# Kernel tuning notes

Hardware: AMD Instinct MI355X
Metric: run time of the kernel (lower is better)

## Reference

```python
import jax, jax.numpy as jnp
import numpy as np

NBITS = 1
GROUP_SIZE = 64
OUT_F = 4096
IN_F = 4096


def setup_inputs() -> dict:
    key = jax.random.key(0)
    k1, k2, k3, k4, k5 = jax.random.split(key, 5)
    x = jax.random.normal(k1, (8192, IN_F), dtype=jnp.float32)
    # packed 1-bit weights: 8 bits per byte, stored as int32 in [0,256)
    W_packed = jax.random.randint(k2, (OUT_F, IN_F // 8), 0, 256, dtype=jnp.int32)
    n_groups = OUT_F * IN_F // GROUP_SIZE
    scale = jax.random.uniform(k3, (n_groups, 1), dtype=jnp.float32) * 0.02 + 0.005
    zero = jax.random.normal(k4, (n_groups, 1), dtype=jnp.float32) * 0.5
    bias = jax.random.normal(k5, (OUT_F,), dtype=jnp.float32) * 0.02
    return {"x": x, "W_packed": W_packed, "scale": scale, "zero": zero, "bias": bias}


def _unpack_1bit(W_packed):
    # (out, in//8) int -> (out, in) float bits, bit 0 first within each byte
    bits = (W_packed[..., None] >> jnp.arange(8, dtype=jnp.int32)) & 1  # (out, in//8, 8)
    return bits.reshape(W_packed.shape[0], -1).astype(jnp.float32)      # (out, in)


def _dequantise(W_packed, scale, zero):
    W_q = _unpack_1bit(W_packed)                       # (out, in)
    W_grouped = W_q.reshape(-1, GROUP_SIZE)            # (n_groups, group_size), axis=1 grouping
    W_hat = (W_grouped - zero) * scale                 # per-group affine dequant
    return W_hat.reshape(OUT_F, IN_F)


def reference(x, W_packed, scale, zero, bias):
    W_hat = _dequantise(W_packed, scale, zero)
    # F.linear: x @ W_hat.T + bias
    return jnp.dot(x, W_hat.T) + bias
```

## Files before the change

kernel.cpp:

```cpp
#include <hip/hip_runtime.h>
#include <hip/hip_bf16.h>

#define IN_F   4096
#define OUT_F  4096

typedef __bf16 bf16;
typedef __attribute__((ext_vector_type(8))) __bf16 bf16x8;
typedef __attribute__((ext_vector_type(4))) __bf16 bf16x4;
typedef __attribute__((ext_vector_type(4))) float floatx4;

__global__ __launch_bounds__(256) void convert_x_kernel(
    const float* __restrict__ x, bf16* __restrict__ xb)
{
    const size_t i = (size_t)blockIdx.x * 256 + threadIdx.x;
    float4 v = ((const float4*)x)[i];
    bf16x4 b = { (bf16)v.x, (bf16)v.y, (bf16)v.z, (bf16)v.w };
    ((bf16x4*)xb)[i] = b;
}

__global__ __launch_bounds__(256) void dequant_w_kernel(
    const int* __restrict__ Wp, const float* __restrict__ scale,
    const float* __restrict__ zero, bf16* __restrict__ Wb)
{
    const int tid = blockIdx.x * 256 + threadIdx.x;
    const int n = tid >> 9;
    const int b = tid & 511;
    const int g = (n << 6) + (b >> 3);
    const float sc = scale[g];
    const float zp = zero[g];
    const bf16 hi = (bf16)((1.0f - zp) * sc);
    const bf16 lo = (bf16)((0.0f - zp) * sc);
    const int v = Wp[tid];
    bf16x8 w;
#pragma unroll
    for (int j = 0; j < 8; ++j) w[j] = ((v >> j) & 1) ? hi : lo;
    *(bf16x8*)&Wb[(size_t)tid * 8] = w;
}

__device__ __forceinline__ void gload_lds16(const void* g, void* l) {
    __builtin_amdgcn_global_load_lds(
        (const __attribute__((address_space(1))) unsigned int*)g,
        (__attribute__((address_space(3))) unsigned int*)l, 16, 0, 0);
}

__global__ __launch_bounds__(256) void bf16_gemm_bt_kernel(
    const bf16* __restrict__ A,
    const bf16* __restrict__ B,
    const float* __restrict__ bias,
    float* __restrict__ out)
{
    __shared__ __align__(16) bf16 as[128 * 64];
    __shared__ __align__(16) bf16 bs[128 * 64];

    const int t      = threadIdx.x;
    const int lane   = t & 63;
    const int wave   = t >> 6;
    const int lane16 = lane & 15;
    const int kq     = lane >> 4;
    const int wm     = wave >> 1;
    const int wn     = wave & 1;

    const int n0 = blockIdx.x * 128;
    const int m0 = blockIdx.y * 128;

    floatx4 acc[4][4];
#pragma unroll
    for (int i = 0; i < 4; ++i)
#pragma unroll
        for (int j = 0; j < 4; ++j)
            acc[i][j] = (floatx4){0.f, 0.f, 0.f, 0.f};

    const int srow8 = lane >> 3;
    const int sunit = lane & 7;

    for (int kt = 0; kt < IN_F / 64; ++kt) {
#pragma unroll
        for (int i = 0; i < 4; ++i) {
            const int row   = wave * 32 + i * 8 + srow8;
            const int gunit = sunit ^ (row & 7);
            gload_lds16(A + (size_t)(m0 + row) * IN_F + kt * 64 + gunit * 8,
                        &as[(wave * 32 + i * 8) * 64]);
            gload_lds16(B + (size_t)(n0 + row) * IN_F + kt * 64 + gunit * 8,
                        &bs[(wave * 32 + i * 8) * 64]);
        }
        __syncthreads();

#pragma unroll
        for (int ks = 0; ks < 2; ++ks) {
            const int u = ks * 4 + kq;
            bf16x8 af[4], bfr[4];
#pragma unroll
            for (int i = 0; i < 4; ++i) {
                const int r = wm * 64 + i * 16 + lane16;
                af[i] = *(const bf16x8*)&as[r * 64 + (u ^ (r & 7)) * 8];
            }
#pragma unroll
            for (int j = 0; j < 4; ++j) {
                const int r = wn * 64 + j * 16 + lane16;
                bfr[j] = *(const bf16x8*)&bs[r * 64 + (u ^ (r & 7)) * 8];
            }
#pragma unroll
            for (int i = 0; i < 4; ++i)
#pragma unroll
                for (int j = 0; j < 4; ++j)
                    acc[i][j] = __builtin_amdgcn_mfma_f32_16x16x32_bf16(
                        af[i], bfr[j], acc[i][j], 0, 0, 0);
        }
        __syncthreads();
    }

#pragma unroll
    for (int j = 0; j < 4; ++j) {
        const int col = n0 + wn * 64 + j * 16 + lane16;
        const float bv = bias[col];
#pragma unroll
        for (int i = 0; i < 4; ++i) {
            const int row = m0 + wm * 64 + i * 16 + kq * 4;
#pragma unroll
            for (int r = 0; r < 4; ++r)
                out[(size_t)(row + r) * OUT_F + col] = acc[i][j][r] + bv;
        }
    }
}

#define SA 72
#define SB 72
__global__ __launch_bounds__(256) void hqq_gemm_fused_kernel(
    const float* __restrict__ x, const int* __restrict__ Wp,
    const float* __restrict__ scale, const float* __restrict__ zero,
    const float* __restrict__ bias, float* __restrict__ out)
{
    __shared__ __align__(16) bf16 asmem[128 * SA];
    __shared__ __align__(16) bf16 bsmem[128 * SB];
    const int t = threadIdx.x, lane = t & 63, wave = t >> 6;
    const int lane16 = lane & 15, kq = lane >> 4;
    const int wm = wave >> 1, wn = wave & 1;
    const int n0 = blockIdx.x * 128, m0 = blockIdx.y * 128;
    floatx4 acc[4][4];
#pragma unroll
    for (int i = 0; i < 4; ++i)
#pragma unroll
        for (int j = 0; j < 4; ++j) acc[i][j] = (floatx4){0.f, 0.f, 0.f, 0.f};
    const int a_col4 = t & 15, a_row0 = t >> 4;
    const int b_nl = t >> 1, b_half = t & 1;
    for (int kt = 0; kt < IN_F / 64; ++kt) {
        const float* xp = x + (size_t)(m0 + a_row0) * IN_F + kt * 64 + a_col4 * 4;
#pragma unroll
        for (int p = 0; p < 8; ++p) {
            float4 v = *(const float4*)(xp + (size_t)(p * 16) * IN_F);
            bf16x4 b = { (bf16)v.x, (bf16)v.y, (bf16)v.z, (bf16)v.w };
            *(bf16x4*)&asmem[(a_row0 + p * 16) * SA + a_col4 * 4] = b;
        }
        {
            const int4 v = *(const int4*)(Wp + (size_t)(n0 + b_nl) * (IN_F / 8)
                                          + kt * 8 + b_half * 4);
            const int g = (n0 + b_nl) * (IN_F / 64) + kt;
            const float sc = scale[g], zp = zero[g];
            const bf16 hi = (bf16)((1.0f - zp) * sc), lo = (bf16)(0.0f - zp * sc);
            const int vals[4] = {v.x, v.y, v.z, v.w};
#pragma unroll
            for (int e = 0; e < 4; ++e) {
                bf16x8 w;
#pragma unroll
                for (int j = 0; j < 8; ++j) w[j] = ((vals[e] >> j) & 1) ? hi : lo;
                *(bf16x8*)&bsmem[b_nl * SB + b_half * 32 + e * 8] = w;
            }
        }
        __syncthreads();
#pragma unroll
        for (int ks = 0; ks < 2; ++ks) {
            bf16x8 af[4], bfr[4];
#pragma unroll
            for (int i = 0; i < 4; ++i)
                af[i] = *(const bf16x8*)&asmem[(wm * 64 + i * 16 + lane16) * SA + ks * 32 + kq * 8];
#pragma unroll
            for (int j = 0; j < 4; ++j)
                bfr[j] = *(const bf16x8*)&bsmem[(wn * 64 + j * 16 + lane16) * SB + ks * 32 + kq * 8];
#pragma unroll
            for (int i = 0; i < 4; ++i)
#pragma unroll
                for (int j = 0; j < 4; ++j)
                    acc[i][j] = __builtin_amdgcn_mfma_f32_16x16x32_bf16(af[i], bfr[j], acc[i][j], 0, 0, 0);
        }
        __syncthreads();
    }
#pragma unroll
    for (int j = 0; j < 4; ++j) {
        const int col = n0 + wn * 64 + j * 16 + lane16;
        const float bv = bias[col];
#pragma unroll
        for (int i = 0; i < 4; ++i) {
            const int row = m0 + wm * 64 + i * 16 + kq * 4;
#pragma unroll
            for (int r = 0; r < 4; ++r)
                out[(size_t)(row + r) * OUT_F + col] = acc[i][j][r] + bv;
        }
    }
}

extern "C" void kernel_launch(void* const* d_in, const int* in_sizes, int n_in,
                              void* d_out, int out_size, void* d_ws, size_t ws_size,
                              hipStream_t stream) {
    const float* x     = (const float*)d_in[0];
    const int*   Wp    = (const int*)d_in[1];
    const float* scale = (const float*)d_in[2];
    const float* zero  = (const float*)d_in[3];
    const float* bias  = (const float*)d_in[4];
    float*       out   = (float*)d_out;

    const int M = in_sizes[0] / IN_F;
    const size_t need = (size_t)M * IN_F * 2 + (size_t)OUT_F * IN_F * 2;

    if (ws_size >= need) {
        bf16* xb = (bf16*)d_ws;
        bf16* Wb = (bf16*)((char*)d_ws + (size_t)M * IN_F * 2);

        convert_x_kernel<<<(M * IN_F / 4) / 256, 256, 0, stream>>>(x, xb);
        dequant_w_kernel<<<(OUT_F * IN_F / 8) / 256, 256, 0, stream>>>(Wp, scale, zero, Wb);

        dim3 grid(OUT_F / 128, M / 128);
        bf16_gemm_bt_kernel<<<grid, 256, 0, stream>>>(xb, Wb, bias, out);
    } else {
        dim3 grid(OUT_F / 128, M / 128);
        hqq_gemm_fused_kernel<<<grid, 256, 0, stream>>>(x, Wp, scale, zero, bias, out);
    }
}
```

Before: 523.2 us.

## Switch GEMM to 32x32x16 MFMA and merge prep kernels into one launch

The bf16 GEMM inner loop now issues 32x32x16 MFMA instructions on 2x2 tiles per wave instead of 16x16x32 on 4x4 tiles. This needs fewer LDS fragment reads per k-step and fewer instructions to issue. The activation conversion and weight dequantisation kernels are merged into a single launch that branches on block index, saving one launch. The epilogue store mapping is rewritten for the 32x32 accumulator layout, and output stores are less contiguous per wave.

```diff
diff --git a/kernel.cpp b/kernel.cpp
--- a/kernel.cpp
+++ b/kernel.cpp
@@ -5,36 +5,36 @@
 #define OUT_F  4096
 
 typedef __bf16 bf16;
-typedef __attribute__((ext_vector_type(8))) __bf16 bf16x8;
-typedef __attribute__((ext_vector_type(4))) __bf16 bf16x4;
-typedef __attribute__((ext_vector_type(4))) float floatx4;
-
-__global__ __launch_bounds__(256) void convert_x_kernel(
-    const float* __restrict__ x, bf16* __restrict__ xb)
+typedef __attribute__((ext_vector_type(8)))  __bf16 bf16x8;
+typedef __attribute__((ext_vector_type(4)))  __bf16 bf16x4;
+typedef __attribute__((ext_vector_type(4)))  float  floatx4;
+typedef __attribute__((ext_vector_type(16))) float  floatx16;
+
+__global__ __launch_bounds__(256) void prep_kernel(
+    const float* __restrict__ x,  bf16* __restrict__ xb,
+    const int* __restrict__ Wp,   const float* __restrict__ scale,
+    const float* __restrict__ zero, bf16* __restrict__ Wb, int nxb)
 {
-    const size_t i = (size_t)blockIdx.x * 256 + threadIdx.x;
-    float4 v = ((const float4*)x)[i];
-    bf16x4 b = { (bf16)v.x, (bf16)v.y, (bf16)v.z, (bf16)v.w };
-    ((bf16x4*)xb)[i] = b;
-}
-
-__global__ __launch_bounds__(256) void dequant_w_kernel(
-    const int* __restrict__ Wp, const float* __restrict__ scale,
-    const float* __restrict__ zero, bf16* __restrict__ Wb)
-{
-    const int tid = blockIdx.x * 256 + threadIdx.x;
-    const int n = tid >> 9;
-    const int b = tid & 511;
-    const int g = (n << 6) + (b >> 3);
-    const float sc = scale[g];
-    const float zp = zero[g];
-    const bf16 hi = (bf16)((1.0f - zp) * sc);
-    const bf16 lo = (bf16)((0.0f - zp) * sc);
-    const int v = Wp[tid];
-    bf16x8 w;
-#pragma unroll
-    for (int j = 0; j < 8; ++j) w[j] = ((v >> j) & 1) ? hi : lo;
-    *(bf16x8*)&Wb[(size_t)tid * 8] = w;
+    if ((int)blockIdx.x < nxb) {
+        const size_t i = (size_t)blockIdx.x * 256 + threadIdx.x;
+        float4 v = ((const float4*)x)[i];
+        bf16x4 b = { (bf16)v.x, (bf16)v.y, (bf16)v.z, (bf16)v.w };
+        ((bf16x4*)xb)[i] = b;
+    } else {
+        const int tid = (blockIdx.x - nxb) * 256 + threadIdx.x;
+        const int n = tid >> 9;
+        const int b = tid & 511;
+        const int g = (n << 6) + (b >> 3);
+        const float sc = scale[g];
+        const float zp = zero[g];
+        const bf16 hi = (bf16)((1.0f - zp) * sc);
+        const bf16 lo = (bf16)((0.0f - zp) * sc);
+        const int v = Wp[tid];
+        bf16x8 w;
+#pragma unroll
+        for (int j = 0; j < 8; ++j) w[j] = ((v >> j) & 1) ? hi : lo;
+        *(bf16x8*)&Wb[(size_t)tid * 8] = w;
+    }
 }
 
 __device__ __forceinline__ void gload_lds16(const void* g, void* l) {
@@ -55,20 +55,21 @@
     const int t      = threadIdx.x;
     const int lane   = t & 63;
     const int wave   = t >> 6;
-    const int lane16 = lane & 15;
-    const int kq     = lane >> 4;
+    const int lane32 = lane & 31;
+    const int half   = lane >> 5;
     const int wm     = wave >> 1;
     const int wn     = wave & 1;
 
     const int n0 = blockIdx.x * 128;
     const int m0 = blockIdx.y * 128;
 
-    floatx4 acc[4][4];
-#pragma unroll
-    for (int i = 0; i < 4; ++i)
-#pragma unroll
-        for (int j = 0; j < 4; ++j)
-            acc[i][j] = (floatx4){0.f, 0.f, 0.f, 0.f};
+    floatx16 acc[2][2];
+#pragma unroll
+    for (int i = 0; i < 2; ++i)
+#pragma unroll
+        for (int j = 0; j < 2; ++j)
+#pragma unroll
+            for (int r = 0; r < 16; ++r) acc[i][j][r] = 0.f;
 
     const int srow8 = lane >> 3;
     const int sunit = lane & 7;
@@ -86,39 +87,41 @@
         __syncthreads();
 
 #pragma unroll
-        for (int ks = 0; ks < 2; ++ks) {
-            const int u = ks * 4 + kq;
-            bf16x8 af[4], bfr[4];
-#pragma unroll
-            for (int i = 0; i < 4; ++i) {
-                const int r = wm * 64 + i * 16 + lane16;
+        for (int s = 0; s < 4; ++s) {
+            const int u = s * 2 + half;
+            bf16x8 af[2], bfr[2];
+#pragma unroll
+            for (int i = 0; i < 2; ++i) {
+                const int r = wm * 64 + i * 32 + lane32;
                 af[i] = *(const bf16x8*)&as[r * 64 + (u ^ (r & 7)) * 8];
             }
 #pragma unroll
-            for (int j = 0; j < 4; ++j) {
-                const int r = wn * 64 + j * 16 + lane16;
+            for (int j = 0; j < 2; ++j) {
+                const int r = wn * 64 + j * 32 + lane32;
                 bfr[j] = *(const bf16x8*)&bs[r * 64 + (u ^ (r & 7)) * 8];
             }
 #pragma unroll
-            for (int i = 0; i < 4; ++i)
-#pragma unroll
-                for (int j = 0; j < 4; ++j)
-                    acc[i][j] = __builtin_amdgcn_mfma_f32_16x16x32_bf16(
+            for (int i = 0; i < 2; ++i)
+#pragma unroll
+                for (int j = 0; j < 2; ++j)
+                    acc[i][j] = __builtin_amdgcn_mfma_f32_32x32x16_bf16(
                         af[i], bfr[j], acc[i][j], 0, 0, 0);
         }
         __syncthreads();
     }
 
 #pragma unroll
-    for (int j = 0; j < 4; ++j) {
-        const int col = n0 + wn * 64 + j * 16 + lane16;
+    for (int j = 0; j < 2; ++j) {
+        const int col = n0 + wn * 64 + j * 32 + lane32;
         const float bv = bias[col];
 #pragma unroll
-        for (int i = 0; i < 4; ++i) {
-            const int row = m0 + wm * 64 + i * 16 + kq * 4;
-#pragma unroll
-            for (int r = 0; r < 4; ++r)
-                out[(size_t)(row + r) * OUT_F + col] = acc[i][j][r] + bv;
+        for (int i = 0; i < 2; ++i) {
+            const int rowbase = m0 + wm * 64 + i * 32 + 4 * half;
+#pragma unroll
+            for (int reg = 0; reg < 16; ++reg) {
+                const int row = rowbase + (reg & 3) + 8 * (reg >> 2);
+                out[(size_t)row * OUT_F + col] = acc[i][j][reg] + bv;
+            }
         }
     }
 }
@@ -215,8 +218,9 @@
         bf16* xb = (bf16*)d_ws;
         bf16* Wb = (bf16*)((char*)d_ws + (size_t)M * IN_F * 2);
 
-        convert_x_kernel<<<(M * IN_F / 4) / 256, 256, 0, stream>>>(x, xb);
-        dequant_w_kernel<<<(OUT_F * IN_F / 8) / 256, 256, 0, stream>>>(Wp, scale, zero, Wb);
+        const int nxb = (M * IN_F / 4) / 256;
+        const int nwb = (OUT_F * IN_F / 8) / 256;
+        prep_kernel<<<nxb + nwb, 256, 0, stream>>>(x, xb, Wp, scale, zero, Wb, nxb);
 
         dim3 grid(OUT_F / 128, M / 128);
         bf16_gemm_bt_kernel<<<grid, 256, 0, stream>>>(xb, Wb, bias, out);
```

After: 509.9 us. 2.5% less time.
